# Performance work log

Measured on AMD Instinct MI355X. Metric: run time of the kernel, lower is better.

Reference implementation:

```python
import jax, jax.numpy as jnp
import numpy as np

NUM_Q_HEADS = 16
NUM_KV_HEADS = 4
GROUP_SIZE = NUM_Q_HEADS // NUM_KV_HEADS  # 4
GROUP_DIM = 128                           # head dim, also RoPE dim
THETA = 10000.0


def _rope_cos_sin(num_tokens, dim, dtype):
    # freqs = 1/theta^(2i/d); angles[t, i] = t * freqs[i]
    inv_freq = 1.0 / (THETA ** (jnp.arange(0, dim, 2, dtype=jnp.float32) / dim))
    t = jnp.arange(num_tokens, dtype=jnp.float32)
    angles = jnp.outer(t, inv_freq)  # [N, d/2]
    # broadcast to [N, 1, 1, d/2] to match q/k shape [B, N, gs, kvh, d/2]
    cos = jnp.cos(angles)[:, None, None, :].astype(dtype)
    sin = jnp.sin(angles)[:, None, None, :].astype(dtype)
    return cos, sin


def _apply_rope(x, cos, sin):
    # x: [B, N, gs, kvh, d]; complex rotation on interleaved (even, odd) pairs
    xr = x.reshape(*x.shape[:-1], -1, 2)
    xe, xo = xr[..., 0], xr[..., 1]
    oe = xe * cos - xo * sin
    oo = xe * sin + xo * cos
    return jnp.stack([oe, oo], axis=-1).reshape(x.shape)


def setup_inputs() -> dict:
    key = jax.random.key(0)
    ks = jax.random.split(key, 5)
    B, N, D = 1, 2048, 2048
    KV_D = GROUP_DIM * NUM_KV_HEADS  # 512
    s = 0.02
    return {
        "x": jax.random.normal(ks[0], (B, N, D), dtype=jnp.float32),
        "Wq": jax.random.normal(ks[1], (D, D), dtype=jnp.float32) * s,
        "Wk": jax.random.normal(ks[2], (D, KV_D), dtype=jnp.float32) * s,
        "Wv": jax.random.normal(ks[3], (D, KV_D), dtype=jnp.float32) * s,
        "Wo": jax.random.normal(ks[4], (D, D), dtype=jnp.float32) * s,
    }


def reference(x, Wq, Wk, Wv, Wo):
    B, N, D = x.shape
    d = GROUP_DIM
    # projections
    q = (x @ Wq).reshape(B, N, GROUP_SIZE, NUM_KV_HEADS, d)
    k = (x @ Wk).reshape(B, N, 1, NUM_KV_HEADS, d)
    v = (x @ Wv).reshape(B, N, 1, NUM_KV_HEADS, d)
    # RoPE (interleaved complex rotation)
    cos, sin = _rope_cos_sin(N, d, x.dtype)
    q = _apply_rope(q, cos, sin)
    k = _apply_rope(k, cos, sin)
    # to [B, kvh, gs, N, d] / [B, kvh, N, d]
    q = jnp.transpose(q, (0, 3, 2, 1, 4))        # b k s n d
    k = jnp.transpose(k[:, :, 0], (0, 2, 1, 3))  # b k m d
    v = jnp.transpose(v[:, :, 0], (0, 2, 1, 3))  # b k m d
    scores = jnp.einsum('bksnd,bkmd->bksnm', q, k)
    causal = jnp.tril(jnp.ones((N, N), dtype=bool))
    scores = jnp.where(causal, scores, -jnp.inf)
    weights = jax.nn.softmax(scores / jnp.sqrt(jnp.asarray(d, x.dtype)), axis=-1)
    ctx = jnp.einsum('bksnm,bkmd->bksnd', weights, v)   # [B, kvh, gs, N, d]
    # flatten heads (kvh-major, matching torch flatten(1,2)), then [B, N, D]
    ctx = ctx.reshape(B, NUM_KV_HEADS * GROUP_SIZE, N, d)
    ctx = jnp.transpose(ctx, (0, 2, 1, 3)).reshape(B, N, D)
    return ctx @ Wo
```

## Files before the change

### kernel.cpp

```cpp
#include <hip/hip_runtime.h>

typedef unsigned short u16;
typedef float f32x4 __attribute__((ext_vector_type(4)));
typedef short s16x8 __attribute__((ext_vector_type(8)));
typedef short s16x4 __attribute__((ext_vector_type(4)));

__device__ __forceinline__ u16 f2b(float f) {
  union { float f; unsigned u; } v; v.f = f;
  unsigned r = v.u + 0x7fffu + ((v.u >> 16) & 1u);
  return (u16)(r >> 16);
}
__device__ __forceinline__ float b2f(u16 b) {
  union { unsigned u; float f; } v; v.u = ((unsigned)b) << 16;
  return v.f;
}
__device__ __forceinline__ f32x4 mfma_bf16(s16x8 a, s16x8 b, f32x4 c) {
  return __builtin_amdgcn_mfma_f32_16x16x32_bf16(a, b, c, 0, 0, 0);
}
__device__ __forceinline__ void gl_lds16(const u16* g, u16* l) {
  __builtin_amdgcn_global_load_lds(
      (const __attribute__((address_space(1))) void*)g,
      (__attribute__((address_space(3))) void*)l, 16, 0, 0);
}

__global__ void conv_x(const float* __restrict__ in, u16* __restrict__ out, int n) {
  int i = (blockIdx.x * 256 + threadIdx.x) * 8;
  if (i >= n) return;
  f32x4 a = *(const f32x4*)(in + i);
  f32x4 b = *(const f32x4*)(in + i + 4);
  s16x8 o = {(short)f2b(a.x), (short)f2b(a.y), (short)f2b(a.z), (short)f2b(a.w),
             (short)f2b(b.x), (short)f2b(b.y), (short)f2b(b.z), (short)f2b(b.w)};
  *(s16x8*)(out + i) = o;
}

__global__ void transW(const float* __restrict__ Wq, const float* __restrict__ Wk,
                       const float* __restrict__ Wv, const float* __restrict__ Wo,
                       u16* __restrict__ WqkvT, u16* __restrict__ WoT) {
  __shared__ u16 tile[64][68];
  const int z = blockIdx.z;
  if (z == 1 && blockIdx.x >= 32) return;
  const int ox = blockIdx.x * 64;
  const int oy = blockIdx.y * 64;
  const float* src; int scol, C; u16* dst;
  if (z == 0) {
    if (ox < 2048)      { src = Wq; scol = ox;        C = 2048; }
    else if (ox < 2560) { src = Wk; scol = ox - 2048; C = 512;  }
    else                { src = Wv; scol = ox - 2560; C = 512;  }
    dst = WqkvT;
  } else { src = Wo; scol = ox; C = 2048; dst = WoT; }
  const int t = threadIdx.x, lr = t >> 4, c4 = (t & 15) * 4;
#pragma unroll
  for (int p = 0; p < 4; ++p) {
    int r = p * 16 + lr;
    f32x4 v = *(const f32x4*)(src + (size_t)(oy + r) * C + scol + c4);
    s16x4 pk = {(short)f2b(v.x), (short)f2b(v.y), (short)f2b(v.z), (short)f2b(v.w)};
    *(s16x4*)(&tile[r][c4]) = pk;
  }
  __syncthreads();
#pragma unroll
  for (int q = 0; q < 4; ++q) {
    int oc = q * 16 + lr;
    s16x4 pk = {(short)tile[c4 + 0][oc], (short)tile[c4 + 1][oc],
                (short)tile[c4 + 2][oc], (short)tile[c4 + 3][oc]};
    *(s16x4*)(dst + (size_t)(ox + oc) * 2048 + oy + c4) = pk;
  }
}

__global__ void transpose_v(const u16* __restrict__ qkv, u16* __restrict__ vT) {
  __shared__ u16 tile[64][68];
  const int bx = blockIdx.x * 64;
  const int by = blockIdx.y * 64;
  const int t = threadIdx.x, lr = t >> 4, c4 = (t & 15) * 4;
#pragma unroll
  for (int p = 0; p < 4; ++p) {
    int r = p * 16 + lr;
    s16x4 v = *(const s16x4*)(qkv + (size_t)(by + r) * 3072 + 2560 + bx + c4);
    *(s16x4*)(&tile[r][c4]) = v;
  }
  __syncthreads();
#pragma unroll
  for (int q = 0; q < 4; ++q) {
    int oc = q * 16 + lr;
    s16x4 pk = {(short)tile[c4 + 0][oc], (short)tile[c4 + 1][oc],
                (short)tile[c4 + 2][oc], (short)tile[c4 + 3][oc]};
    *(s16x4*)(vT + (size_t)(bx + oc) * 2048 + by + c4) = pk;
  }
}

__global__ __launch_bounds__(256, 2) void gemm_qkv(const u16* __restrict__ A,
                                                   const u16* __restrict__ Bt,
                                                   u16* __restrict__ C) {
  __shared__ __align__(16) u16 As[64 * 32];
  __shared__ __align__(16) u16 Bs[128 * 32];
  const int K = 2048;
  const int n0 = blockIdx.x * 128, m0 = blockIdx.y * 64;
  const int t = threadIdx.x, wave = t >> 6, lane = t & 63;
  const int quad = lane >> 4, lc = lane & 15;
  const int wm = (wave >> 1) * 32, wn = (wave & 1) * 64;
  const int arow = t >> 2, akc = (t & 3) * 8;

  const f32x4 z = {0.f, 0.f, 0.f, 0.f};
  f32x4 acc[2][4];
#pragma unroll
  for (int i = 0; i < 2; ++i)
#pragma unroll
    for (int j = 0; j < 4; ++j) acc[i][j] = z;

  for (int k0 = 0; k0 < K; k0 += 32) {
    gl_lds16(A  + (size_t)(m0 + arow) * K + k0 + akc, As + wave * 512);
    gl_lds16(Bt + (size_t)(n0 + arow) * K + k0 + akc, Bs + wave * 512);
    gl_lds16(Bt + (size_t)(n0 + 64 + arow) * K + k0 + akc, Bs + 2048 + wave * 512);
    __syncthreads();
    s16x8 af[2], bfr[4];
#pragma unroll
    for (int i = 0; i < 2; ++i)
      af[i] = *(const s16x8*)(As + (wm + i * 16 + lc) * 32 + quad * 8);
#pragma unroll
    for (int j = 0; j < 4; ++j)
      bfr[j] = *(const s16x8*)(Bs + (wn + j * 16 + lc) * 32 + quad * 8);
#pragma unroll
    for (int i = 0; i < 2; ++i)
#pragma unroll
      for (int j = 0; j < 4; ++j)
        acc[i][j] = mfma_bf16(af[i], bfr[j], acc[i][j]);
    __syncthreads();
  }
#pragma unroll
  for (int j = 0; j < 4; ++j) {
    const int colbase = wn + j * 16;
    const bool rope = (n0 + colbase) < 2560;
    const int col = n0 + colbase + lc;
    const int ip = ((colbase + lc) & 127) >> 1;
    const float inv_freq = exp2f(-0.20762050593046014f * (float)ip);
#pragma unroll
    for (int i = 0; i < 2; ++i)
#pragma unroll
      for (int r = 0; r < 4; ++r) {
        float v = acc[i][j][r];
        float p = __shfl_xor(v, 1);
        float val = v;
        if (rope) {
          int token = m0 + wm + i * 16 + quad * 4 + r;
          float ang = (float)token * inv_freq;
          float sv, cv;
          sincosf(ang, &sv, &cv);
          val = (lc & 1) ? (p * sv + v * cv) : (v * cv - p * sv);
        }
        C[(size_t)(m0 + wm + i * 16 + quad * 4 + r) * 3072 + col] = f2b(val);
      }
  }
}

__global__ __launch_bounds__(256, 2) void gemm_out(const u16* __restrict__ A,
                                                   const u16* __restrict__ Bt,
                                                   float* __restrict__ C) {
  __shared__ __align__(16) u16 As[64 * 32];
  __shared__ __align__(16) u16 Bs[128 * 32];
  const int K = 2048;
  const int n0 = blockIdx.x * 128, m0 = blockIdx.y * 64;
  const int t = threadIdx.x, wave = t >> 6, lane = t & 63;
  const int quad = lane >> 4, lc = lane & 15;
  const int wm = (wave >> 1) * 32, wn = (wave & 1) * 64;
  const int arow = t >> 2, akc = (t & 3) * 8;

  const f32x4 z = {0.f, 0.f, 0.f, 0.f};
  f32x4 acc[2][4];
#pragma unroll
  for (int i = 0; i < 2; ++i)
#pragma unroll
    for (int j = 0; j < 4; ++j) acc[i][j] = z;

  for (int k0 = 0; k0 < K; k0 += 32) {
    gl_lds16(A  + (size_t)(m0 + arow) * K + k0 + akc, As + wave * 512);
    gl_lds16(Bt + (size_t)(n0 + arow) * K + k0 + akc, Bs + wave * 512);
    gl_lds16(Bt + (size_t)(n0 + 64 + arow) * K + k0 + akc, Bs + 2048 + wave * 512);
    __syncthreads();
    s16x8 af[2], bfr[4];
#pragma unroll
    for (int i = 0; i < 2; ++i)
      af[i] = *(const s16x8*)(As + (wm + i * 16 + lc) * 32 + quad * 8);
#pragma unroll
    for (int j = 0; j < 4; ++j)
      bfr[j] = *(const s16x8*)(Bs + (wn + j * 16 + lc) * 32 + quad * 8);
#pragma unroll
    for (int i = 0; i < 2; ++i)
#pragma unroll
      for (int j = 0; j < 4; ++j)
        acc[i][j] = mfma_bf16(af[i], bfr[j], acc[i][j]);
    __syncthreads();
  }
#pragma unroll
  for (int i = 0; i < 2; ++i)
#pragma unroll
    for (int j = 0; j < 4; ++j)
#pragma unroll
      for (int r = 0; r < 4; ++r)
        C[(size_t)(m0 + wm + i * 16 + quad * 4 + r) * 2048 + n0 + wn + j * 16 + lc] =
            acc[i][j][r];
}

__global__ __launch_bounds__(256, 2) void attn_k(const u16* __restrict__ qkv,
                                                 const u16* __restrict__ vT,
                                                 u16* __restrict__ Opart,
                                                 float* __restrict__ Lpart) {
  const int qt = blockIdx.x, hq = blockIdx.y, half = blockIdx.z;
  const int kvh = hq & 3, sg = hq >> 2;
  const int qc0 = hq << 7, kc0 = 2048 + (kvh << 7), vr0 = kvh << 7;

  __shared__ __align__(16) u16 Qs[64 * 136];
  __shared__ __align__(16) u16 Ks[64 * 136];
  __shared__ __align__(16) u16 Vs[128 * 72];
  __shared__ __align__(16) u16 Ps[64 * 72];

  const int t = threadIdx.x, wave = t >> 6, lane = t & 63;
  const int quad = lane >> 4, lc = lane & 15;
  const int kr = t >> 4, kc = (t & 15) * 8;
  const int vr = t >> 3, vc = (t & 7) * 8;

  {
#pragma unroll
    for (int p = 0; p < 4; ++p)
      *(s16x8*)(Qs + (p * 16 + kr) * 136 + kc) =
          *(const s16x8*)(qkv + (size_t)(qt * 64 + p * 16 + kr) * 3072 + qc0 + kc);
  }

  const f32x4 z = {0.f, 0.f, 0.f, 0.f};
  f32x4 oa[8];
#pragma unroll
  for (int n = 0; n < 8; ++n) oa[n] = z;
  float Ls[4] = {0.f, 0.f, 0.f, 0.f};
  const float scale2 = 0.12751744545f;
  const int qrow_base = qt * 64 + wave * 16 + quad * 4;

  const int ntiles = qt + 1, n0t = (ntiles + 1) >> 1;
  const int lo = half ? n0t : 0, hi = half ? ntiles : n0t;

  s16x8 kreg[4], vreg[4];
  if (lo < hi) {
    const int j0 = lo * 64;
#pragma unroll
    for (int p = 0; p < 4; ++p)
      kreg[p] = *(const s16x8*)(qkv + (size_t)(j0 + p * 16 + kr) * 3072 + kc0 + kc);
#pragma unroll
    for (int p = 0; p < 4; ++p)
      vreg[p] = *(const s16x8*)(vT + (size_t)(vr0 + p * 32 + vr) * 2048 + j0 + vc);
  }

  for (int tile = lo; tile < hi; ++tile) {
    const int j0 = tile * 64;
    __syncthreads();
#pragma unroll
    for (int p = 0; p < 4; ++p)
      *(s16x8*)(Ks + (p * 16 + kr) * 136 + kc) = kreg[p];
#pragma unroll
    for (int p = 0; p < 4; ++p)
      *(s16x8*)(Vs + (p * 32 + vr) * 72 + vc) = vreg[p];
    if (tile + 1 < hi) {
      const int j1 = j0 + 64;
#pragma unroll
      for (int p = 0; p < 4; ++p)
        kreg[p] = *(const s16x8*)(qkv + (size_t)(j1 + p * 16 + kr) * 3072 + kc0 + kc);
#pragma unroll
      for (int p = 0; p < 4; ++p)
        vreg[p] = *(const s16x8*)(vT + (size_t)(vr0 + p * 32 + vr) * 2048 + j1 + vc);
    }
    __syncthreads();
    f32x4 sa[4];
#pragma unroll
    for (int n = 0; n < 4; ++n) sa[n] = z;
#pragma unroll
    for (int ks = 0; ks < 4; ++ks) {
      s16x8 af = *(const s16x8*)(Qs + (wave * 16 + lc) * 136 + ks * 32 + quad * 8);
#pragma unroll
      for (int n = 0; n < 4; ++n) {
        s16x8 bf = *(const s16x8*)(Ks + (n * 16 + lc) * 136 + ks * 32 + quad * 8);
        sa[n] = mfma_bf16(af, bf, sa[n]);
      }
    }
#pragma unroll
    for (int n = 0; n < 4; ++n) {
      int jc = j0 + n * 16 + lc;
#pragma unroll
      for (int r = 0; r < 4; ++r) {
        float e = (jc <= qrow_base + r) ? exp2f(sa[n][r] * scale2) : 0.f;
        Ps[(wave * 16 + quad * 4 + r) * 72 + n * 16 + lc] = f2b(e);
        Ls[r] += e;
      }
    }
#pragma unroll
    for (int ks = 0; ks < 2; ++ks) {
      s16x8 af = *(const s16x8*)(Ps + (wave * 16 + lc) * 72 + ks * 32 + quad * 8);
#pragma unroll
      for (int n = 0; n < 8; ++n) {
        s16x8 bf = *(const s16x8*)(Vs + (n * 16 + lc) * 72 + ks * 32 + quad * 8);
        oa[n] = mfma_bf16(af, bf, oa[n]);
      }
    }
  }
#pragma unroll
  for (int r = 0; r < 4; ++r) {
    float s = Ls[r];
    s += __shfl_xor(s, 1);
    s += __shfl_xor(s, 2);
    s += __shfl_xor(s, 4);
    s += __shfl_xor(s, 8);
    Ls[r] = s;
  }
  const size_t tbase = (size_t)(half * 16 + hq) * 32 + qt;
  u16* Ob = Opart + tbase * (64 * 128);
  if (lc == 0) {
#pragma unroll
    for (int r = 0; r < 4; ++r)
      Lpart[tbase * 64 + wave * 16 + quad * 4 + r] = Ls[r];
  }
#pragma unroll
  for (int n = 0; n < 8; ++n)
#pragma unroll
    for (int r = 0; r < 4; ++r)
      Ob[(wave * 16 + quad * 4 + r) * 128 + n * 16 + lc] = f2b(oa[n][r]);
}

__global__ void attn_combine(const u16* __restrict__ Opart,
                             const float* __restrict__ Lpart,
                             u16* __restrict__ ctx) {
  const int hq = blockIdx.y, kvh = hq & 3, sg = hq >> 2;
  const int lin = blockIdx.x * 256 + threadIdx.x;
  const int token = lin >> 4, d8 = (lin & 15) << 3;
  const int qt = token >> 6, row = token & 63;
  const size_t t0 = (size_t)hq * 32 + qt, t1 = t0 + 512;
  const u16* O0 = Opart + t0 * 8192 + row * 128 + d8;
  const u16* O1 = Opart + t1 * 8192 + row * 128 + d8;
  const float inv = 1.f / (Lpart[t0 * 64 + row] + Lpart[t1 * 64 + row]);
  s16x8 a = *(const s16x8*)O0, b = *(const s16x8*)O1;
  s16x8 o;
#pragma unroll
  for (int i = 0; i < 8; ++i)
    o[i] = (short)f2b((b2f((u16)a[i]) + b2f((u16)b[i])) * inv);
  *(s16x8*)(ctx + (size_t)token * 2048 + ((kvh * 4 + sg) << 7) + d8) = o;
}

extern "C" void kernel_launch(void* const* d_in, const int* in_sizes, int n_in,
                              void* d_out, int out_size, void* d_ws, size_t ws_size,
                              hipStream_t stream) {
  const float* x  = (const float*)d_in[0];
  const float* Wq = (const float*)d_in[1];
  const float* Wk = (const float*)d_in[2];
  const float* Wv = (const float*)d_in[3];
  const float* Wo = (const float*)d_in[4];

  char* w = (char*)d_ws;
  u16* xb     = (u16*)w;  w += (size_t)2048 * 2048 * 2;
  u16* WqkvT  = (u16*)w;  w += (size_t)3072 * 2048 * 2;
  u16* WoT    = (u16*)w;  w += (size_t)2048 * 2048 * 2;
  u16* qkvb   = (u16*)w;  w += (size_t)2048 * 3072 * 2;
  u16* vTb    = (u16*)w;  w += (size_t)512 * 2048 * 2;
  u16* ctxb   = (u16*)w;  w += (size_t)2048 * 2048 * 2;
  float* Lpart= (float*)w; w += (size_t)2 * 16 * 32 * 64 * 4;
  u16* Opart  = (u16*)d_ws;

  conv_x<<<2048, 256, 0, stream>>>(x, xb, 2048 * 2048);
  transW<<<dim3(48, 32, 2), 256, 0, stream>>>(Wq, Wk, Wv, Wo, WqkvT, WoT);

  gemm_qkv<<<dim3(24, 32), 256, 0, stream>>>(xb, WqkvT, qkvb);

  transpose_v<<<dim3(8, 32), 256, 0, stream>>>(qkvb, vTb);

  attn_k<<<dim3(32, 16, 2), 256, 0, stream>>>(qkvb, vTb, Opart, Lpart);
  attn_combine<<<dim3(128, 16), 256, 0, stream>>>(Opart, Lpart, ctxb);

  gemm_out<<<dim3(16, 32), 256, 0, stream>>>(ctxb, WoT, (float*)d_out);
}
```

Measured before the change: 263.1 us.

## Load Q and K fragments directly into registers; double-buffer V in LDS

The attention kernel now keeps the Q fragments in registers for the whole kernel. Each wave reads its K MFMA fragments straight from global memory every tile instead of staging K through LDS. V is double-buffered in shared memory, which cuts the loop to one barrier per tile and shrinks LDS use. The cost is that every wave fetches the full K tile, so global/L2 traffic for K is four times higher. That K load is also not prefetched, so its latency sits right in front of the QK MFMAs, and the extra registers may lower occupancy.

```diff
diff --git a/kernel.cpp b/kernel.cpp
--- a/kernel.cpp
+++ b/kernel.cpp
@@ -207,22 +207,18 @@
   const int kvh = hq & 3, sg = hq >> 2;
   const int qc0 = hq << 7, kc0 = 2048 + (kvh << 7), vr0 = kvh << 7;
 
-  __shared__ __align__(16) u16 Qs[64 * 136];
-  __shared__ __align__(16) u16 Ks[64 * 136];
-  __shared__ __align__(16) u16 Vs[128 * 72];
+  __shared__ __align__(16) u16 Vs[2][128 * 72];
   __shared__ __align__(16) u16 Ps[64 * 72];
 
   const int t = threadIdx.x, wave = t >> 6, lane = t & 63;
   const int quad = lane >> 4, lc = lane & 15;
-  const int kr = t >> 4, kc = (t & 15) * 8;
   const int vr = t >> 3, vc = (t & 7) * 8;
 
-  {
-#pragma unroll
-    for (int p = 0; p < 4; ++p)
-      *(s16x8*)(Qs + (p * 16 + kr) * 136 + kc) =
-          *(const s16x8*)(qkv + (size_t)(qt * 64 + p * 16 + kr) * 3072 + qc0 + kc);
-  }
+  s16x8 qf[4];
+#pragma unroll
+  for (int ks = 0; ks < 4; ++ks)
+    qf[ks] = *(const s16x8*)(qkv + (size_t)(qt * 64 + wave * 16 + lc) * 3072 +
+                             qc0 + ks * 32 + quad * 8);
 
   const f32x4 z = {0.f, 0.f, 0.f, 0.f};
   f32x4 oa[8];
@@ -235,48 +231,41 @@
   const int ntiles = qt + 1, n0t = (ntiles + 1) >> 1;
   const int lo = half ? n0t : 0, hi = half ? ntiles : n0t;
 
-  s16x8 kreg[4], vreg[4];
+  s16x8 vreg[4];
   if (lo < hi) {
     const int j0 = lo * 64;
 #pragma unroll
     for (int p = 0; p < 4; ++p)
-      kreg[p] = *(const s16x8*)(qkv + (size_t)(j0 + p * 16 + kr) * 3072 + kc0 + kc);
+      vreg[p] = *(const s16x8*)(vT + (size_t)(vr0 + p * 32 + vr) * 2048 + j0 + vc);
 #pragma unroll
     for (int p = 0; p < 4; ++p)
-      vreg[p] = *(const s16x8*)(vT + (size_t)(vr0 + p * 32 + vr) * 2048 + j0 + vc);
-  }
+      *(s16x8*)(Vs[lo & 1] + (p * 32 + vr) * 72 + vc) = vreg[p];
+  }
+  __syncthreads();
 
   for (int tile = lo; tile < hi; ++tile) {
     const int j0 = tile * 64;
-    __syncthreads();
-#pragma unroll
-    for (int p = 0; p < 4; ++p)
-      *(s16x8*)(Ks + (p * 16 + kr) * 136 + kc) = kreg[p];
-#pragma unroll
-    for (int p = 0; p < 4; ++p)
-      *(s16x8*)(Vs + (p * 32 + vr) * 72 + vc) = vreg[p];
     if (tile + 1 < hi) {
-      const int j1 = j0 + 64;
 #pragma unroll
       for (int p = 0; p < 4; ++p)
-        kreg[p] = *(const s16x8*)(qkv + (size_t)(j1 + p * 16 + kr) * 3072 + kc0 + kc);
-#pragma unroll
-      for (int p = 0; p < 4; ++p)
-        vreg[p] = *(const s16x8*)(vT + (size_t)(vr0 + p * 32 + vr) * 2048 + j1 + vc);
+        vreg[p] = *(const s16x8*)(vT + (size_t)(vr0 + p * 32 + vr) * 2048 +
+                                  j0 + 64 + vc);
     }
-    __syncthreads();
+    s16x8 kf[16];
+#pragma unroll
+    for (int ks = 0; ks < 4; ++ks)
+#pragma unroll
+      for (int n = 0; n < 4; ++n)
+        kf[ks * 4 + n] = *(const s16x8*)(qkv + (size_t)(j0 + n * 16 + lc) * 3072 +
+                                         kc0 + ks * 32 + quad * 8);
     f32x4 sa[4];
 #pragma unroll
     for (int n = 0; n < 4; ++n) sa[n] = z;
 #pragma unroll
-    for (int ks = 0; ks < 4; ++ks) {
-      s16x8 af = *(const s16x8*)(Qs + (wave * 16 + lc) * 136 + ks * 32 + quad * 8);
-#pragma unroll
-      for (int n = 0; n < 4; ++n) {
-        s16x8 bf = *(const s16x8*)(Ks + (n * 16 + lc) * 136 + ks * 32 + quad * 8);
-        sa[n] = mfma_bf16(af, bf, sa[n]);
-      }
-    }
+    for (int ks = 0; ks < 4; ++ks)
+#pragma unroll
+      for (int n = 0; n < 4; ++n)
+        sa[n] = mfma_bf16(qf[ks], kf[ks * 4 + n], sa[n]);
 #pragma unroll
     for (int n = 0; n < 4; ++n) {
       int jc = j0 + n * 16 + lc;
@@ -287,15 +276,22 @@
         Ls[r] += e;
       }
     }
+    const u16* Vb = Vs[tile & 1];
 #pragma unroll
     for (int ks = 0; ks < 2; ++ks) {
       s16x8 af = *(const s16x8*)(Ps + (wave * 16 + lc) * 72 + ks * 32 + quad * 8);
 #pragma unroll
       for (int n = 0; n < 8; ++n) {
-        s16x8 bf = *(const s16x8*)(Vs + (n * 16 + lc) * 72 + ks * 32 + quad * 8);
+        s16x8 bf = *(const s16x8*)(Vb + (n * 16 + lc) * 72 + ks * 32 + quad * 8);
         oa[n] = mfma_bf16(af, bf, oa[n]);
       }
     }
+    if (tile + 1 < hi) {
+#pragma unroll
+      for (int p = 0; p < 4; ++p)
+        *(s16x8*)(Vs[(tile + 1) & 1] + (p * 32 + vr) * 72 + vc) = vreg[p];
+    }
+    __syncthreads();
   }
 #pragma unroll
   for (int r = 0; r < 4; ++r) {
```

Result: slower. 328.0 us (+24.6%).

## Enlarge GEMM tiles to 128x128 and rebalance causal attention with variable KV splits

Applied to the files above, without the earlier changes.

Both GEMMs now use a shared core with 128x128 block tiles and a 4x4 MFMA accumulator per wave, raising register-level reuse and halving the grid size. Attention processes 128-row query tiles with Q held in registers, and splits the causal KV range into 1-4 chunks of 8 tiles depending on query position, giving 40 balanced blocks per head instead of a fixed two-way split. The combine kernel sums a variable number of partials. The workspace layout is reshuffled so Opart overlaps the xb/WqkvT buffers, which are dead by the time attention runs. Costs are more registers per thread, possible occupancy loss, and fewer blocks for the GEMMs on a large GPU.

```diff
diff --git a/kernel.cpp b/kernel.cpp
--- a/kernel.cpp
+++ b/kernel.cpp
@@ -87,44 +87,53 @@
   }
 }
 
+__device__ __forceinline__ void gemm_core(const u16* __restrict__ A,
+                                          const u16* __restrict__ Bt,
+                                          int K, int m0, int n0,
+                                          f32x4 (*acc)[4], u16* As, u16* Bs) {
+  const int t = threadIdx.x;
+  const int wave = t >> 6, lane = t & 63, quad = lane >> 4, lc = lane & 15;
+  const int wm = (wave >> 1) * 64, wn = (wave & 1) * 64;
+  for (int k0 = 0; k0 < K; k0 += 32) {
+#pragma unroll
+    for (int h = 0; h < 2; ++h) {
+      int ch = h * 256 + t, row = ch >> 2, kc = (ch & 3) * 8;
+      gl_lds16(A  + (size_t)(m0 + row) * K + k0 + kc, As + (size_t)(h * 256 + wave * 64) * 8);
+      gl_lds16(Bt + (size_t)(n0 + row) * K + k0 + kc, Bs + (size_t)(h * 256 + wave * 64) * 8);
+    }
+    __syncthreads();
+    s16x8 af[4], bfr[4];
+#pragma unroll
+    for (int i = 0; i < 4; ++i)
+      af[i] = *(const s16x8*)(As + (wm + i * 16 + lc) * 32 + quad * 8);
+#pragma unroll
+    for (int j = 0; j < 4; ++j)
+      bfr[j] = *(const s16x8*)(Bs + (wn + j * 16 + lc) * 32 + quad * 8);
+#pragma unroll
+    for (int i = 0; i < 4; ++i)
+#pragma unroll
+      for (int j = 0; j < 4; ++j)
+        acc[i][j] = mfma_bf16(af[i], bfr[j], acc[i][j]);
+    __syncthreads();
+  }
+}
+
 __global__ __launch_bounds__(256, 2) void gemm_qkv(const u16* __restrict__ A,
                                                    const u16* __restrict__ Bt,
                                                    u16* __restrict__ C) {
-  __shared__ __align__(16) u16 As[64 * 32];
+  __shared__ __align__(16) u16 As[128 * 32];
   __shared__ __align__(16) u16 Bs[128 * 32];
-  const int K = 2048;
-  const int n0 = blockIdx.x * 128, m0 = blockIdx.y * 64;
-  const int t = threadIdx.x, wave = t >> 6, lane = t & 63;
+  const int n0 = blockIdx.x * 128, m0 = blockIdx.y * 128;
+  const int lane = threadIdx.x & 63, wave = threadIdx.x >> 6;
   const int quad = lane >> 4, lc = lane & 15;
-  const int wm = (wave >> 1) * 32, wn = (wave & 1) * 64;
-  const int arow = t >> 2, akc = (t & 3) * 8;
-
+  const int wm = (wave >> 1) * 64, wn = (wave & 1) * 64;
   const f32x4 z = {0.f, 0.f, 0.f, 0.f};
-  f32x4 acc[2][4];
-#pragma unroll
-  for (int i = 0; i < 2; ++i)
+  f32x4 acc[4][4];
+#pragma unroll
+  for (int i = 0; i < 4; ++i)
 #pragma unroll
     for (int j = 0; j < 4; ++j) acc[i][j] = z;
-
-  for (int k0 = 0; k0 < K; k0 += 32) {
-    gl_lds16(A  + (size_t)(m0 + arow) * K + k0 + akc, As + wave * 512);
-    gl_lds16(Bt + (size_t)(n0 + arow) * K + k0 + akc, Bs + wave * 512);
-    gl_lds16(Bt + (size_t)(n0 + 64 + arow) * K + k0 + akc, Bs + 2048 + wave * 512);
-    __syncthreads();
-    s16x8 af[2], bfr[4];
-#pragma unroll
-    for (int i = 0; i < 2; ++i)
-      af[i] = *(const s16x8*)(As + (wm + i * 16 + lc) * 32 + quad * 8);
-#pragma unroll
-    for (int j = 0; j < 4; ++j)
-      bfr[j] = *(const s16x8*)(Bs + (wn + j * 16 + lc) * 32 + quad * 8);
-#pragma unroll
-    for (int i = 0; i < 2; ++i)
-#pragma unroll
-      for (int j = 0; j < 4; ++j)
-        acc[i][j] = mfma_bf16(af[i], bfr[j], acc[i][j]);
-    __syncthreads();
-  }
+  gemm_core(A, Bt, 2048, m0, n0, acc, As, Bs);
 #pragma unroll
   for (int j = 0; j < 4; ++j) {
     const int colbase = wn + j * 16;
@@ -133,7 +142,7 @@
     const int ip = ((colbase + lc) & 127) >> 1;
     const float inv_freq = exp2f(-0.20762050593046014f * (float)ip);
 #pragma unroll
-    for (int i = 0; i < 2; ++i)
+    for (int i = 0; i < 4; ++i)
 #pragma unroll
       for (int r = 0; r < 4; ++r) {
         float v = acc[i][j][r];
@@ -154,43 +163,21 @@
 __global__ __launch_bounds__(256, 2) void gemm_out(const u16* __restrict__ A,
                                                    const u16* __restrict__ Bt,
                                                    float* __restrict__ C) {
-  __shared__ __align__(16) u16 As[64 * 32];
+  __shared__ __align__(16) u16 As[128 * 32];
   __shared__ __align__(16) u16 Bs[128 * 32];
-  const int K = 2048;
-  const int n0 = blockIdx.x * 128, m0 = blockIdx.y * 64;
-  const int t = threadIdx.x, wave = t >> 6, lane = t & 63;
+  const int n0 = blockIdx.x * 128, m0 = blockIdx.y * 128;
+  const int lane = threadIdx.x & 63, wave = threadIdx.x >> 6;
   const int quad = lane >> 4, lc = lane & 15;
-  const int wm = (wave >> 1) * 32, wn = (wave & 1) * 64;
-  const int arow = t >> 2, akc = (t & 3) * 8;
-
+  const int wm = (wave >> 1) * 64, wn = (wave & 1) * 64;
   const f32x4 z = {0.f, 0.f, 0.f, 0.f};
-  f32x4 acc[2][4];
-#pragma unroll
-  for (int i = 0; i < 2; ++i)
+  f32x4 acc[4][4];
+#pragma unroll
+  for (int i = 0; i < 4; ++i)
 #pragma unroll
     for (int j = 0; j < 4; ++j) acc[i][j] = z;
-
-  for (int k0 = 0; k0 < K; k0 += 32) {
-    gl_lds16(A  + (size_t)(m0 + arow) * K + k0 + akc, As + wave * 512);
-    gl_lds16(Bt + (size_t)(n0 + arow) * K + k0 + akc, Bs + wave * 512);
-    gl_lds16(Bt + (size_t)(n0 + 64 + arow) * K + k0 + akc, Bs + 2048 + wave * 512);
-    __syncthreads();
-    s16x8 af[2], bfr[4];
-#pragma unroll
-    for (int i = 0; i < 2; ++i)
-      af[i] = *(const s16x8*)(As + (wm + i * 16 + lc) * 32 + quad * 8);
-#pragma unroll
-    for (int j = 0; j < 4; ++j)
-      bfr[j] = *(const s16x8*)(Bs + (wn + j * 16 + lc) * 32 + quad * 8);
-#pragma unroll
-    for (int i = 0; i < 2; ++i)
-#pragma unroll
-      for (int j = 0; j < 4; ++j)
-        acc[i][j] = mfma_bf16(af[i], bfr[j], acc[i][j]);
-    __syncthreads();
-  }
-#pragma unroll
-  for (int i = 0; i < 2; ++i)
+  gemm_core(A, Bt, 2048, m0, n0, acc, As, Bs);
+#pragma unroll
+  for (int i = 0; i < 4; ++i)
 #pragma unroll
     for (int j = 0; j < 4; ++j)
 #pragma unroll
@@ -203,121 +190,143 @@
                                                  const u16* __restrict__ vT,
                                                  u16* __restrict__ Opart,
                                                  float* __restrict__ Lpart) {
-  const int qt = blockIdx.x, hq = blockIdx.y, half = blockIdx.z;
-  const int kvh = hq & 3, sg = hq >> 2;
+  const int bid = blockIdx.x;
+  const int hq = bid / 40, idx = bid % 40;
+  int qt, c;
+  if (idx < 4)       { qt = idx;                          c = 0; }
+  else if (idx < 12) { int w = idx - 4;  qt = 4 + (w >> 1);  c = w & 1; }
+  else if (idx < 24) { int w = idx - 12; qt = 8 + w / 3;     c = w % 3; }
+  else               { int w = idx - 24; qt = 12 + (w >> 2); c = w & 3; }
+  const int s0 = c * 8;
+  const int s1 = min(c * 8 + 8, 2 * qt + 2);
+
+  const int kvh = hq & 3;
   const int qc0 = hq << 7, kc0 = 2048 + (kvh << 7), vr0 = kvh << 7;
 
-  __shared__ __align__(16) u16 Qs[64 * 136];
   __shared__ __align__(16) u16 Ks[64 * 136];
   __shared__ __align__(16) u16 Vs[128 * 72];
-  __shared__ __align__(16) u16 Ps[64 * 72];
+  __shared__ __align__(16) u16 Ps[128 * 72];
 
   const int t = threadIdx.x, wave = t >> 6, lane = t & 63;
   const int quad = lane >> 4, lc = lane & 15;
   const int kr = t >> 4, kc = (t & 15) * 8;
   const int vr = t >> 3, vc = (t & 7) * 8;
 
+  s16x8 qf[2][4];
+#pragma unroll
+  for (int i = 0; i < 2; ++i)
+#pragma unroll
+    for (int ks = 0; ks < 4; ++ks)
+      qf[i][ks] = *(const s16x8*)(qkv +
+          (size_t)(qt * 128 + wave * 32 + i * 16 + lc) * 3072 +
+          qc0 + ks * 32 + quad * 8);
+
+  const f32x4 z = {0.f, 0.f, 0.f, 0.f};
+  f32x4 oa[2][8];
+#pragma unroll
+  for (int i = 0; i < 2; ++i)
+#pragma unroll
+    for (int n = 0; n < 8; ++n) oa[i][n] = z;
+  float Ls[2][4] = {{0.f, 0.f, 0.f, 0.f}, {0.f, 0.f, 0.f, 0.f}};
+  const float scale2 = 0.12751744545f;
+
+  s16x8 kpf[4], vpf[4];
   {
+    const int j0 = s0 * 64;
 #pragma unroll
     for (int p = 0; p < 4; ++p)
-      *(s16x8*)(Qs + (p * 16 + kr) * 136 + kc) =
-          *(const s16x8*)(qkv + (size_t)(qt * 64 + p * 16 + kr) * 3072 + qc0 + kc);
-  }
-
-  const f32x4 z = {0.f, 0.f, 0.f, 0.f};
-  f32x4 oa[8];
-#pragma unroll
-  for (int n = 0; n < 8; ++n) oa[n] = z;
-  float Ls[4] = {0.f, 0.f, 0.f, 0.f};
-  const float scale2 = 0.12751744545f;
-  const int qrow_base = qt * 64 + wave * 16 + quad * 4;
-
-  const int ntiles = qt + 1, n0t = (ntiles + 1) >> 1;
-  const int lo = half ? n0t : 0, hi = half ? ntiles : n0t;
-
-  s16x8 kreg[4], vreg[4];
-  if (lo < hi) {
-    const int j0 = lo * 64;
+      kpf[p] = *(const s16x8*)(qkv + (size_t)(j0 + p * 16 + kr) * 3072 + kc0 + kc);
 #pragma unroll
     for (int p = 0; p < 4; ++p)
-      kreg[p] = *(const s16x8*)(qkv + (size_t)(j0 + p * 16 + kr) * 3072 + kc0 + kc);
-#pragma unroll
-    for (int p = 0; p < 4; ++p)
-      vreg[p] = *(const s16x8*)(vT + (size_t)(vr0 + p * 32 + vr) * 2048 + j0 + vc);
-  }
-
-  for (int tile = lo; tile < hi; ++tile) {
+      vpf[p] = *(const s16x8*)(vT + (size_t)(vr0 + p * 32 + vr) * 2048 + j0 + vc);
+  }
+
+  for (int tile = s0; tile < s1; ++tile) {
     const int j0 = tile * 64;
     __syncthreads();
 #pragma unroll
     for (int p = 0; p < 4; ++p)
-      *(s16x8*)(Ks + (p * 16 + kr) * 136 + kc) = kreg[p];
+      *(s16x8*)(Ks + (p * 16 + kr) * 136 + kc) = kpf[p];
 #pragma unroll
     for (int p = 0; p < 4; ++p)
-      *(s16x8*)(Vs + (p * 32 + vr) * 72 + vc) = vreg[p];
-    if (tile + 1 < hi) {
+      *(s16x8*)(Vs + (p * 32 + vr) * 72 + vc) = vpf[p];
+    __syncthreads();
+    if (tile + 1 < s1) {
       const int j1 = j0 + 64;
 #pragma unroll
       for (int p = 0; p < 4; ++p)
-        kreg[p] = *(const s16x8*)(qkv + (size_t)(j1 + p * 16 + kr) * 3072 + kc0 + kc);
+        kpf[p] = *(const s16x8*)(qkv + (size_t)(j1 + p * 16 + kr) * 3072 + kc0 + kc);
 #pragma unroll
       for (int p = 0; p < 4; ++p)
-        vreg[p] = *(const s16x8*)(vT + (size_t)(vr0 + p * 32 + vr) * 2048 + j1 + vc);
+        vpf[p] = *(const s16x8*)(vT + (size_t)(vr0 + p * 32 + vr) * 2048 + j1 + vc);
     }
-    __syncthreads();
-    f32x4 sa[4];
-#pragma unroll
-    for (int n = 0; n < 4; ++n) sa[n] = z;
-#pragma unroll
-    for (int ks = 0; ks < 4; ++ks) {
-      s16x8 af = *(const s16x8*)(Qs + (wave * 16 + lc) * 136 + ks * 32 + quad * 8);
+    f32x4 sa[2][4];
+#pragma unroll
+    for (int i = 0; i < 2; ++i)
+#pragma unroll
+      for (int n = 0; n < 4; ++n) sa[i][n] = z;
+#pragma unroll
+    for (int ks = 0; ks < 4; ++ks)
 #pragma unroll
       for (int n = 0; n < 4; ++n) {
         s16x8 bf = *(const s16x8*)(Ks + (n * 16 + lc) * 136 + ks * 32 + quad * 8);
-        sa[n] = mfma_bf16(af, bf, sa[n]);
+        sa[0][n] = mfma_bf16(qf[0][ks], bf, sa[0][n]);
+        sa[1][n] = mfma_bf16(qf[1][ks], bf, sa[1][n]);
+      }
+#pragma unroll
+    for (int i = 0; i < 2; ++i) {
+      const int qrow_base = qt * 128 + wave * 32 + i * 16 + quad * 4;
+#pragma unroll
+      for (int n = 0; n < 4; ++n) {
+        int jc = j0 + n * 16 + lc;
+#pragma unroll
+        for (int r = 0; r < 4; ++r) {
+          float e = (jc <= qrow_base + r) ? exp2f(sa[i][n][r] * scale2) : 0.f;
+          Ps[(wave * 32 + i * 16 + quad * 4 + r) * 72 + n * 16 + lc] = f2b(e);
+          Ls[i][r] += e;
+        }
       }
     }
 #pragma unroll
-    for (int n = 0; n < 4; ++n) {
-      int jc = j0 + n * 16 + lc;
-#pragma unroll
-      for (int r = 0; r < 4; ++r) {
-        float e = (jc <= qrow_base + r) ? exp2f(sa[n][r] * scale2) : 0.f;
-        Ps[(wave * 16 + quad * 4 + r) * 72 + n * 16 + lc] = f2b(e);
-        Ls[r] += e;
+    for (int ks = 0; ks < 2; ++ks)
+#pragma unroll
+      for (int i = 0; i < 2; ++i) {
+        s16x8 af = *(const s16x8*)(Ps + (wave * 32 + i * 16 + lc) * 72 +
+                                   ks * 32 + quad * 8);
+#pragma unroll
+        for (int n = 0; n < 8; ++n) {
+          s16x8 bf = *(const s16x8*)(Vs + (n * 16 + lc) * 72 + ks * 32 + quad * 8);
+          oa[i][n] = mfma_bf16(af, bf, oa[i][n]);
+        }
       }
+  }
+#pragma unroll
+  for (int i = 0; i < 2; ++i)
+#pragma unroll
+    for (int r = 0; r < 4; ++r) {
+      float s = Ls[i][r];
+      s += __shfl_xor(s, 1);
+      s += __shfl_xor(s, 2);
+      s += __shfl_xor(s, 4);
+      s += __shfl_xor(s, 8);
+      Ls[i][r] = s;
     }
-#pragma unroll
-    for (int ks = 0; ks < 2; ++ks) {
-      s16x8 af = *(const s16x8*)(Ps + (wave * 16 + lc) * 72 + ks * 32 + quad * 8);
-#pragma unroll
-      for (int n = 0; n < 8; ++n) {
-        s16x8 bf = *(const s16x8*)(Vs + (n * 16 + lc) * 72 + ks * 32 + quad * 8);
-        oa[n] = mfma_bf16(af, bf, oa[n]);
-      }
-    }
-  }
-#pragma unroll
-  for (int r = 0; r < 4; ++r) {
-    float s = Ls[r];
-    s += __shfl_xor(s, 1);
-    s += __shfl_xor(s, 2);
-    s += __shfl_xor(s, 4);
-    s += __shfl_xor(s, 8);
-    Ls[r] = s;
-  }
-  const size_t tbase = (size_t)(half * 16 + hq) * 32 + qt;
-  u16* Ob = Opart + tbase * (64 * 128);
+  u16* Ob = Opart + (size_t)bid * (128 * 128);
   if (lc == 0) {
 #pragma unroll
-    for (int r = 0; r < 4; ++r)
-      Lpart[tbase * 64 + wave * 16 + quad * 4 + r] = Ls[r];
-  }
-#pragma unroll
-  for (int n = 0; n < 8; ++n)
-#pragma unroll
-    for (int r = 0; r < 4; ++r)
-      Ob[(wave * 16 + quad * 4 + r) * 128 + n * 16 + lc] = f2b(oa[n][r]);
+    for (int i = 0; i < 2; ++i)
+#pragma unroll
+      for (int r = 0; r < 4; ++r)
+        Lpart[(size_t)bid * 128 + wave * 32 + i * 16 + quad * 4 + r] = Ls[i][r];
+  }
+#pragma unroll
+  for (int i = 0; i < 2; ++i)
+#pragma unroll
+    for (int n = 0; n < 8; ++n)
+#pragma unroll
+      for (int r = 0; r < 4; ++r)
+        Ob[(wave * 32 + i * 16 + quad * 4 + r) * 128 + n * 16 + lc] =
+            f2b(oa[i][n][r]);
 }
 
 __global__ void attn_combine(const u16* __restrict__ Opart,
@@ -326,17 +335,25 @@
   const int hq = blockIdx.y, kvh = hq & 3, sg = hq >> 2;
   const int lin = blockIdx.x * 256 + threadIdx.x;
   const int token = lin >> 4, d8 = (lin & 15) << 3;
-  const int qt = token >> 6, row = token & 63;
-  const size_t t0 = (size_t)hq * 32 + qt, t1 = t0 + 512;
-  const u16* O0 = Opart + t0 * 8192 + row * 128 + d8;
-  const u16* O1 = Opart + t1 * 8192 + row * 128 + d8;
-  const float inv = 1.f / (Lpart[t0 * 64 + row] + Lpart[t1 * 64 + row]);
-  s16x8 a = *(const s16x8*)O0, b = *(const s16x8*)O1;
-  s16x8 o;
-#pragma unroll
-  for (int i = 0; i < 8; ++i)
-    o[i] = (short)f2b((b2f((u16)a[i]) + b2f((u16)b[i])) * inv);
-  *(s16x8*)(ctx + (size_t)token * 2048 + ((kvh * 4 + sg) << 7) + d8) = o;
+  const int qt = token >> 7, row = token & 127;
+  const int tier = qt >> 2;
+  const int btab[4] = {0, 4, 12, 24};
+  const int base = hq * 40 + btab[tier] + (qt & 3) * (tier + 1);
+  const int cnt = tier + 1;
+  float acc[8] = {0.f, 0.f, 0.f, 0.f, 0.f, 0.f, 0.f, 0.f};
+  float L = 0.f;
+  for (int c = 0; c < cnt; ++c) {
+    const int b = base + c;
+    L += Lpart[(size_t)b * 128 + row];
+    s16x8 o = *(const s16x8*)(Opart + (size_t)b * 16384 + row * 128 + d8);
+#pragma unroll
+    for (int i = 0; i < 8; ++i) acc[i] += b2f((u16)o[i]);
+  }
+  const float inv = 1.f / L;
+  s16x8 out;
+#pragma unroll
+  for (int i = 0; i < 8; ++i) out[i] = (short)f2b(acc[i] * inv);
+  *(s16x8*)(ctx + (size_t)token * 2048 + ((kvh * 4 + sg) << 7) + d8) = out;
 }
 
 extern "C" void kernel_launch(void* const* d_in, const int* in_sizes, int n_in,
@@ -349,24 +366,25 @@
   const float* Wo = (const float*)d_in[4];
 
   char* w = (char*)d_ws;
+  u16* qkvb   = (u16*)w;  w += (size_t)2048 * 3072 * 2;
+  u16* vTb    = (u16*)w;  w += (size_t)512 * 2048 * 2;
+  u16* WoT    = (u16*)w;  w += (size_t)2048 * 2048 * 2;
+  u16* ctxb   = (u16*)w;  w += (size_t)2048 * 2048 * 2;
+  float* Lpart= (float*)w; w += (size_t)640 * 128 * 4;
+  u16* Opart  = (u16*)w;
   u16* xb     = (u16*)w;  w += (size_t)2048 * 2048 * 2;
   u16* WqkvT  = (u16*)w;  w += (size_t)3072 * 2048 * 2;
-  u16* WoT    = (u16*)w;  w += (size_t)2048 * 2048 * 2;
-  u16* qkvb   = (u16*)w;  w += (size_t)2048 * 3072 * 2;
-  u16* vTb    = (u16*)w;  w += (size_t)512 * 2048 * 2;
-  u16* ctxb   = (u16*)w;  w += (size_t)2048 * 2048 * 2;
-  float* Lpart= (float*)w; w += (size_t)2 * 16 * 32 * 64 * 4;
-  u16* Opart  = (u16*)d_ws;
+  w += (size_t)2 * 1024 * 1024;
 
   conv_x<<<2048, 256, 0, stream>>>(x, xb, 2048 * 2048);
   transW<<<dim3(48, 32, 2), 256, 0, stream>>>(Wq, Wk, Wv, Wo, WqkvT, WoT);
 
-  gemm_qkv<<<dim3(24, 32), 256, 0, stream>>>(xb, WqkvT, qkvb);
+  gemm_qkv<<<dim3(24, 16), 256, 0, stream>>>(xb, WqkvT, qkvb);
 
   transpose_v<<<dim3(8, 32), 256, 0, stream>>>(qkvb, vTb);
 
-  attn_k<<<dim3(32, 16, 2), 256, 0, stream>>>(qkvb, vTb, Opart, Lpart);
+  attn_k<<<640, 256, 0, stream>>>(qkvb, vTb, Opart, Lpart);
   attn_combine<<<dim3(128, 16), 256, 0, stream>>>(Opart, Lpart, ctxb);
 
-  gemm_out<<<dim3(16, 32), 256, 0, stream>>>(ctxb, WoT, (float*)d_out);
-}
+  gemm_out<<<dim3(16, 16), 256, 0, stream>>>(ctxb, WoT, (float*)d_out);
+}
```

Result: faster. 253.2 us (-3.8%).
